# Kernel optimization log

Hardware: AMD Instinct MI355X
Metric: run time of the kernel (lower is better)

The kernel has to match this reference:

```python
import jax, jax.numpy as jnp
import numpy as np

S, B, D, E = 257, 64, 768, 8
H = 4 * D  # expert hidden dim

def quick_gelu(x):
    return x * jax.nn.sigmoid(1.702 * x)

def setup_inputs() -> dict:
    key = jax.random.key(0)
    ks = jax.random.split(key, 7)
    scale = 1.0 / np.sqrt(D)
    return {
        "x": jax.random.normal(ks[0], (S, B, D), dtype=jnp.float32),
        "W1": jax.random.normal(ks[1], (E, H, D), dtype=jnp.float32) * scale,   # fc1 weight per expert (out,in)
        "b1": jax.random.normal(ks[2], (E, H), dtype=jnp.float32) * 0.01,
        "W2": jax.random.normal(ks[3], (E, D, H), dtype=jnp.float32) * (1.0 / np.sqrt(H)),
        "b2": jax.random.normal(ks[4], (E, D), dtype=jnp.float32) * 0.01,
        "Wr": jax.random.normal(ks[5], (E, D), dtype=jnp.float32) * scale,       # router weight (E, d)
        "br": jnp.zeros((E,), dtype=jnp.float32),
    }

def reference(x, W1, b1, W2, b2, Wr, br):
    s, b, d = x.shape
    xf = x.reshape(s * b, d)                                  # [T, d]
    logits = xf @ Wr.T + br                                   # [T, E]
    probs = jax.nn.softmax(logits, axis=-1)                   # [T, E]
    # all-experts MLP, batched over the expert axis
    h = jnp.einsum('td,ehd->teh', xf, W1) + b1                # [T, E, 4d]
    h = quick_gelu(h)
    outs = jnp.einsum('teh,edh->ted', h, W2) + b2             # [T, E, d]
    y = jnp.einsum('ted,te->td', outs, probs)                 # router-weighted combine
    return y.reshape(s, b, d)
```

## Files before the change

kernel.cpp:

```cpp
#include <hip/hip_runtime.h>

typedef unsigned short u16;
typedef float f32x4 __attribute__((ext_vector_type(4)));
typedef short s16x8 __attribute__((ext_vector_type(8)));

#define T_TOK   16448L
#define D_DIM   768L
#define H_DIM   3072L
#define E_NUM   8L
#define M_PAD   16512L

__device__ __forceinline__ u16 f2bf(float f){
  unsigned u = __float_as_uint(f);
  u = u + 0x7FFFu + ((u >> 16) & 1u);
  return (u16)(u >> 16);
}
__device__ __forceinline__ unsigned f2bf2(float a, float b){
  return (unsigned)f2bf(a) | ((unsigned)f2bf(b) << 16);
}

__device__ __forceinline__ void gload_lds16(const u16* g, u16* s){
  __builtin_amdgcn_global_load_lds((const __attribute__((address_space(1))) void*)g,
                                   (__attribute__((address_space(3))) void*)s,
                                   16, 0, 0);
}

__device__ __forceinline__ int xcd_chunk(int idx, int n){
  const int q = n >> 3, r = n & 7, x = idx & 7;
  return (x < r ? x*(q+1) : r*(q+1) + (x-r)*q) + (idx >> 3);
}

__global__ void k_conv(const float* __restrict__ in, u16* __restrict__ outp,
                       long nValid, long nTotal){
  long i = (long)blockIdx.x * blockDim.x + threadIdx.x;
  long stride = (long)gridDim.x * blockDim.x;
  long n8 = nTotal >> 3;
  for (long v = i; v < n8; v += stride){
    long base = v << 3;
    uint4 o;
    if (base < nValid){
      const float4 f0 = *(const float4*)(in + base);
      const float4 f1 = *(const float4*)(in + base + 4);
      o.x = f2bf2(f0.x, f0.y); o.y = f2bf2(f0.z, f0.w);
      o.z = f2bf2(f1.x, f1.y); o.w = f2bf2(f1.z, f1.w);
    } else {
      o.x = 0u; o.y = 0u; o.z = 0u; o.w = 0u;
    }
    *(uint4*)(outp + base) = o;
  }
}

__global__ void k_router(const float* __restrict__ x, const float* __restrict__ Wr,
                         const float* __restrict__ br, float* __restrict__ probs){
  int w = (int)((blockIdx.x * (long)blockDim.x + threadIdx.x) >> 6);
  int lane = threadIdx.x & 63;
  if (w >= (int)T_TOK) return;
  const float* xr = x + (long)w * D_DIM;
  float l[8];
#pragma unroll
  for (int e = 0; e < 8; ++e) l[e] = 0.f;
#pragma unroll
  for (int c = 0; c < 3; ++c){
    const float4 xv = *(const float4*)(xr + c*256 + lane*4);
#pragma unroll
    for (int e = 0; e < 8; ++e){
      const float4 wv = *(const float4*)(Wr + (long)e*D_DIM + c*256 + lane*4);
      l[e] += xv.x*wv.x + xv.y*wv.y + xv.z*wv.z + xv.w*wv.w;
    }
  }
#pragma unroll
  for (int e = 0; e < 8; ++e){
#pragma unroll
    for (int off = 32; off > 0; off >>= 1) l[e] += __shfl_xor(l[e], off);
    l[e] += br[e];
  }
  float m = l[0];
#pragma unroll
  for (int e = 1; e < 8; ++e) m = fmaxf(m, l[e]);
  float s = 0.f;
#pragma unroll
  for (int e = 0; e < 8; ++e){ l[e] = __expf(l[e] - m); s += l[e]; }
  float inv = 1.f / s;
  if (lane == 0){
    float4 p0 = { l[0]*inv, l[1]*inv, l[2]*inv, l[3]*inv };
    float4 p1 = { l[4]*inv, l[5]*inv, l[6]*inv, l[7]*inv };
    *(float4*)(probs + (long)w*8)     = p0;
    *(float4*)(probs + (long)w*8 + 4) = p1;
  }
}

__device__ __forceinline__ void gemm128(const u16* __restrict__ Ag, long lda,
                                        const u16* __restrict__ Bg, long ldb,
                                        int NT, u16* As, u16* Bs,
                                        int tid, f32x4 (&acc)[4][4]){
  const int l  = tid & 63, w = tid >> 6;
  const int wr = w >> 1,  wc = w & 1;
  const int g4 = l >> 4,  ln = l & 15;

  const int rw = l >> 3;
  const int c8 = (l & 7) ^ rw;
  const u16* pA = Ag + (long)(w*8 + rw) * lda + c8*8;
  const u16* pB = Bg + (long)(w*8 + rw) * ldb + c8*8;
  const long sA = 32 * lda, sB = 32 * ldb;
  u16* dA = As + w*512;
  u16* dB = Bs + w*512;

  int offA[2][4], offB[2][4];
#pragma unroll
  for (int kk = 0; kk < 2; ++kk)
#pragma unroll
    for (int i = 0; i < 4; ++i){
      const int co = (((kk<<2) | g4) ^ (ln & 7)) << 3;
      offA[kk][i] = (wr*64 + i*16 + ln)*64 + co;
      offB[kk][i] = (wc*64 + i*16 + ln)*64 + co;
    }

  for (int kt = 0; kt < NT; ++kt){
    gload_lds16(pA,        dA);
    gload_lds16(pA +   sA, dA + 2048);
    gload_lds16(pA + 2*sA, dA + 4096);
    gload_lds16(pA + 3*sA, dA + 6144);
    gload_lds16(pB,        dB);
    gload_lds16(pB +   sB, dB + 2048);
    gload_lds16(pB + 2*sB, dB + 4096);
    gload_lds16(pB + 3*sB, dB + 6144);
    pA += 64; pB += 64;
    __syncthreads();

    s16x8 a0[4], b0[4], a1[4], b1[4];
#pragma unroll
    for (int i = 0; i < 4; ++i) a0[i] = *(const s16x8*)(As + offA[0][i]);
#pragma unroll
    for (int i = 0; i < 4; ++i) b0[i] = *(const s16x8*)(Bs + offB[0][i]);
#pragma unroll
    for (int mi = 0; mi < 4; ++mi)
#pragma unroll
      for (int ni = 0; ni < 4; ++ni)
        acc[mi][ni] = __builtin_amdgcn_mfma_f32_16x16x32_bf16(a0[mi], b0[ni], acc[mi][ni], 0, 0, 0);
#pragma unroll
    for (int i = 0; i < 4; ++i) a1[i] = *(const s16x8*)(As + offA[1][i]);
#pragma unroll
    for (int i = 0; i < 4; ++i) b1[i] = *(const s16x8*)(Bs + offB[1][i]);
#pragma unroll
    for (int mi = 0; mi < 4; ++mi)
#pragma unroll
      for (int ni = 0; ni < 4; ++ni)
        acc[mi][ni] = __builtin_amdgcn_mfma_f32_16x16x32_bf16(a1[mi], b1[ni], acc[mi][ni], 0, 0, 0);
    __syncthreads();
  }
}

__global__ __launch_bounds__(256) void k_pair(const u16* __restrict__ xb,
                                              const u16* __restrict__ w1b,
                                              const float* __restrict__ b1,
                                              const u16* __restrict__ w2b,
                                              const float* __restrict__ b2,
                                              const float* __restrict__ probs,
                                              float* __restrict__ out,
                                              const u16* __restrict__ hbR,
                                              u16* __restrict__ hbW,
                                              int e2, int t02,
                                              int e1, int t01, int mt1, int n2){
  __shared__ alignas(16) u16 As[8192];
  __shared__ alignas(16) u16 Bs[8192];
  const int tid = threadIdx.x;
  const int l  = tid & 63, w = tid >> 6;
  const int wr = w >> 1,  wc = w & 1;
  const int g4 = l >> 4,  ln = l & 15;
  const int bx = (int)blockIdx.x;
  f32x4 acc[4][4] = {};

  if (bx < n2){
    const int wg = xcd_chunk(bx, n2);
    const int tx = wg / 6, ty = wg % 6;
    const int m0 = tx << 7, n0 = ty << 7;
    gemm128(hbR + (long)m0 * H_DIM, H_DIM,
            w2b + ((long)e2 * D_DIM + n0) * H_DIM, H_DIM,
            48, As, Bs, tid, acc);
    float bias[4];
#pragma unroll
    for (int ni = 0; ni < 4; ++ni) bias[ni] = b2[(long)e2*D_DIM + n0 + wc*64 + ni*16 + ln];
#pragma unroll
    for (int mi = 0; mi < 4; ++mi){
#pragma unroll
      for (int j = 0; j < 4; ++j){
        const int gt = t02 + m0 + wr*64 + mi*16 + g4*4 + j;
        if (gt < (int)T_TOK){
          const float p = probs[(long)gt*8 + e2];
          float* dst = out + (long)gt * D_DIM + n0 + wc*64;
#pragma unroll
          for (int ni = 0; ni < 4; ++ni){
            const float v = p * (acc[mi][ni][j] + bias[ni]);
            if (e2 == 0) dst[ni*16 + ln] = v;
            else         dst[ni*16 + ln] += v;
          }
        }
      }
    }
  } else {
    const int n1 = (int)gridDim.x - n2;
    const int wg = xcd_chunk(bx - n2, n1);
    const int tx = wg % mt1, ty = wg / mt1;
    const int m0 = tx << 7, n0 = ty << 7;
    gemm128(xb + (long)(t01 + m0) * D_DIM, D_DIM,
            w1b + ((long)e1 * H_DIM + n0) * D_DIM, D_DIM,
            12, As, Bs, tid, acc);
    float bias[4];
#pragma unroll
    for (int ni = 0; ni < 4; ++ni) bias[ni] = b1[(long)e1*H_DIM + n0 + wc*64 + ni*16 + ln];
#pragma unroll
    for (int mi = 0; mi < 4; ++mi){
#pragma unroll
      for (int j = 0; j < 4; ++j){
        const int r = m0 + wr*64 + mi*16 + g4*4 + j;
        u16* dst = hbW + (long)r * H_DIM + n0 + wc*64;
#pragma unroll
        for (int ni = 0; ni < 4; ++ni){
          const float v  = acc[mi][ni][j] + bias[ni];
          const float gl = v / (1.0f + __expf(-1.702f * v));
          dst[ni*16 + ln] = f2bf(gl);
        }
      }
    }
  }
}

extern "C" void kernel_launch(void* const* d_in, const int* in_sizes, int n_in,
                              void* d_out, int out_size, void* d_ws, size_t ws_size,
                              hipStream_t stream){
  const float* x  = (const float*)d_in[0];
  const float* W1 = (const float*)d_in[1];
  const float* b1 = (const float*)d_in[2];
  const float* W2 = (const float*)d_in[3];
  const float* b2 = (const float*)d_in[4];
  const float* Wr = (const float*)d_in[5];
  const float* br = (const float*)d_in[6];
  float* out = (float*)d_out;

  char* ws = (char*)d_ws;
  size_t off = 0;
  auto carve = [&](size_t bytes)->void*{
    void* p = ws + off; off += (bytes + 255) & ~(size_t)255; return p;
  };
  u16*   xb    = (u16*)  carve((size_t)M_PAD * D_DIM * 2);
  u16*   w1b   = (u16*)  carve((size_t)E_NUM * H_DIM * D_DIM * 2);
  u16*   w2b   = (u16*)  carve((size_t)E_NUM * D_DIM * H_DIM * 2);
  float* probs = (float*)carve((size_t)T_TOK * E_NUM * 4);
  u16*   hbA   = (u16*)  carve((size_t)8192 * H_DIM * 2);
  u16*   hbB   = (u16*)  carve((size_t)8320 * H_DIM * 2);

  k_conv<<<dim3(2048), dim3(256), 0, stream>>>(x,  xb,  T_TOK*D_DIM, M_PAD*D_DIM);
  k_conv<<<dim3(2048), dim3(256), 0, stream>>>(W1, w1b, E_NUM*H_DIM*D_DIM, E_NUM*H_DIM*D_DIM);
  k_conv<<<dim3(2048), dim3(256), 0, stream>>>(W2, w2b, E_NUM*D_DIM*H_DIM, E_NUM*D_DIM*H_DIM);
  k_router<<<dim3(4112), dim3(256), 0, stream>>>(x, Wr, br, probs);

  const int MTA = 64, MTB = 65;
  const int T0A = 0,  T0B = 8192;

  auto pair = [&](int e2, const u16* hbR, int t02, int mt2,
                  int e1, u16* hbW, int t01, int mt1){
    const int n2 = mt2 * 6, n1 = mt1 * 24;
    k_pair<<<dim3((unsigned)(n2 + n1)), dim3(256), 0, stream>>>(
        xb, w1b, b1, w2b, b2, probs, out, hbR, hbW,
        e2, t02, e1, t01, mt1, n2);
  };

  pair(0, nullptr, 0, 0, 0, hbA, T0A, MTA);
  for (int e = 0; e < 8; ++e){
    pair(e, hbA, T0A, MTA, e, hbB, T0B, MTB);
    if (e < 7) pair(e, hbB, T0B, MTB, e + 1, hbA, T0A, MTA);
  }
  pair(7, hbB, T0B, MTB, 0, nullptr, 0, 0);
}
```

Before: 2.110 ms.

## Replace per-expert kernel launches with persistent megakernel using atomic flag dependencies

Merges the sequence of 17 paired GEMM launches into one large grid. Blocks are ordered by expert and role, and they wait on global atomic counters: fc1 waits until the previous expert's fc2 has finished reading the buffer, fc2 waits for fc1 to complete, and per-tile tickets order the output accumulation. A new init kernel zeroes the output and the flags. The aim is to remove launch gaps and tail idle time between kernels so the two phases overlap. The cost is spin-waiting, a dependence on blocks being dispatched in order (deadlock risk otherwise), and serialized output read-modify-write.

After: 4.271 ms. +102.4%, slower.

```diff
diff --git a/kernel.cpp b/kernel.cpp
--- a/kernel.cpp
+++ b/kernel.cpp
@@ -10,6 +10,12 @@
 #define E_NUM   8L
 #define M_PAD   16512L
 
+#define G1A 1536
+#define G2A 384
+#define G1B 1560
+#define G2B 390
+#define PE  3872
+
 __device__ __forceinline__ u16 f2bf(float f){
   unsigned u = __float_as_uint(f);
   u = u + 0x7FFFu + ((u >> 16) & 1u);
@@ -28,6 +34,35 @@
 __device__ __forceinline__ int xcd_chunk(int idx, int n){
   const int q = n >> 3, r = n & 7, x = idx & 7;
   return (x < r ? x*(q+1) : r*(q+1) + (x-r)*q) + (idx >> 3);
+}
+
+__device__ __forceinline__ void spin_ge(const int* p, int need){
+  if (threadIdx.x == 0){
+    while (__hip_atomic_load(p, __ATOMIC_RELAXED, __HIP_MEMORY_SCOPE_AGENT) < need)
+      __builtin_amdgcn_s_sleep(16);
+  }
+  __syncthreads();
+  __builtin_amdgcn_fence(__ATOMIC_ACQUIRE, "agent");
+}
+__device__ __forceinline__ void spin_eq(const int* p, int want){
+  if (threadIdx.x == 0){
+    while (__hip_atomic_load(p, __ATOMIC_RELAXED, __HIP_MEMORY_SCOPE_AGENT) != want)
+      __builtin_amdgcn_s_sleep(16);
+  }
+  __syncthreads();
+  __builtin_amdgcn_fence(__ATOMIC_ACQUIRE, "agent");
+}
+__device__ __forceinline__ void signal_add(int* p){
+  __syncthreads();
+  if (threadIdx.x == 0)
+    __hip_atomic_fetch_add(p, 1, __ATOMIC_RELEASE, __HIP_MEMORY_SCOPE_AGENT);
+}
+
+__global__ void k_init(float* __restrict__ out, long n, int* __restrict__ flags, int nf){
+  long i = (long)blockIdx.x * blockDim.x + threadIdx.x;
+  long st = (long)gridDim.x * blockDim.x;
+  for (long v = i; v < n; v += st) out[v] = 0.f;
+  for (long v = i; v < nf; v += st) flags[v] = 0;
 }
 
 __global__ void k_conv(const float* __restrict__ in, u16* __restrict__ outp,
@@ -150,70 +185,57 @@
   }
 }
 
-__global__ __launch_bounds__(256) void k_pair(const u16* __restrict__ xb,
+__global__ __launch_bounds__(256) void k_mega(const u16* __restrict__ xb,
                                               const u16* __restrict__ w1b,
                                               const float* __restrict__ b1,
                                               const u16* __restrict__ w2b,
                                               const float* __restrict__ b2,
                                               const float* __restrict__ probs,
                                               float* __restrict__ out,
-                                              const u16* __restrict__ hbR,
-                                              u16* __restrict__ hbW,
-                                              int e2, int t02,
-                                              int e1, int t01, int mt1, int n2){
+                                              u16* __restrict__ hbA,
+                                              u16* __restrict__ hbB,
+                                              int* __restrict__ flags){
   __shared__ alignas(16) u16 As[8192];
   __shared__ alignas(16) u16 Bs[8192];
   const int tid = threadIdx.x;
   const int l  = tid & 63, w = tid >> 6;
   const int wr = w >> 1,  wc = w & 1;
   const int g4 = l >> 4,  ln = l & 15;
-  const int bx = (int)blockIdx.x;
+
+  const int e = (int)blockIdx.x / PE;
+  const int r = (int)blockIdx.x % PE;
+  if (r >= 3870) return;
+  int* cnt    = flags;
+  int* gdone  = flags + 16;
+  int* ticket = flags + 32;
+
+  int role, half, wg;
+  if      (r < G1A)            { role = 1; half = 0; wg = xcd_chunk(r, G1A); }
+  else if (r < G1A+G2A)        { role = 2; half = 0; wg = xcd_chunk(r - G1A, G2A); }
+  else if (r < G1A+G2A+G1B)    { role = 1; half = 1; wg = xcd_chunk(r - G1A - G2A, G1B); }
+  else                         { role = 2; half = 1; wg = xcd_chunk(r - G1A - G2A - G1B, G2B); }
+
   f32x4 acc[4][4] = {};
 
-  if (bx < n2){
-    const int wg = xcd_chunk(bx, n2);
-    const int tx = wg / 6, ty = wg % 6;
-    const int m0 = tx << 7, n0 = ty << 7;
-    gemm128(hbR + (long)m0 * H_DIM, H_DIM,
-            w2b + ((long)e2 * D_DIM + n0) * H_DIM, H_DIM,
-            48, As, Bs, tid, acc);
-    float bias[4];
-#pragma unroll
-    for (int ni = 0; ni < 4; ++ni) bias[ni] = b2[(long)e2*D_DIM + n0 + wc*64 + ni*16 + ln];
-#pragma unroll
-    for (int mi = 0; mi < 4; ++mi){
-#pragma unroll
-      for (int j = 0; j < 4; ++j){
-        const int gt = t02 + m0 + wr*64 + mi*16 + g4*4 + j;
-        if (gt < (int)T_TOK){
-          const float p = probs[(long)gt*8 + e2];
-          float* dst = out + (long)gt * D_DIM + n0 + wc*64;
-#pragma unroll
-          for (int ni = 0; ni < 4; ++ni){
-            const float v = p * (acc[mi][ni][j] + bias[ni]);
-            if (e2 == 0) dst[ni*16 + ln] = v;
-            else         dst[ni*16 + ln] += v;
-          }
-        }
-      }
-    }
-  } else {
-    const int n1 = (int)gridDim.x - n2;
-    const int wg = xcd_chunk(bx - n2, n1);
+  if (role == 1){
+    const int mt1 = half ? 65 : 64;
+    const int t01 = half ? 8192 : 0;
+    u16* hbW = half ? hbB : hbA;
     const int tx = wg % mt1, ty = wg / mt1;
     const int m0 = tx << 7, n0 = ty << 7;
+    if (e > 0) spin_ge(&gdone[(e-1)*2 + half], half ? G2B : G2A);
     gemm128(xb + (long)(t01 + m0) * D_DIM, D_DIM,
-            w1b + ((long)e1 * H_DIM + n0) * D_DIM, D_DIM,
+            w1b + ((long)e * H_DIM + n0) * D_DIM, D_DIM,
             12, As, Bs, tid, acc);
     float bias[4];
 #pragma unroll
-    for (int ni = 0; ni < 4; ++ni) bias[ni] = b1[(long)e1*H_DIM + n0 + wc*64 + ni*16 + ln];
+    for (int ni = 0; ni < 4; ++ni) bias[ni] = b1[(long)e*H_DIM + n0 + wc*64 + ni*16 + ln];
 #pragma unroll
     for (int mi = 0; mi < 4; ++mi){
 #pragma unroll
       for (int j = 0; j < 4; ++j){
-        const int r = m0 + wr*64 + mi*16 + g4*4 + j;
-        u16* dst = hbW + (long)r * H_DIM + n0 + wc*64;
+        const int rr = m0 + wr*64 + mi*16 + g4*4 + j;
+        u16* dst = hbW + (long)rr * H_DIM + n0 + wc*64;
 #pragma unroll
         for (int ni = 0; ni < 4; ++ni){
           const float v  = acc[mi][ni][j] + bias[ni];
@@ -222,6 +244,40 @@
         }
       }
     }
+    signal_add(&cnt[e*2 + half]);
+  } else {
+    const int mt2 = half ? 65 : 64;
+    const int t02 = half ? 8192 : 0;
+    const u16* hbR = half ? hbB : hbA;
+    const int tx = wg / 6, ty = wg % 6;
+    const int m0 = tx << 7, n0 = ty << 7;
+    spin_ge(&cnt[e*2 + half], half ? G1B : G1A);
+    gemm128(hbR + (long)m0 * H_DIM, H_DIM,
+            w2b + ((long)e * D_DIM + n0) * H_DIM, H_DIM,
+            48, As, Bs, tid, acc);
+    signal_add(&gdone[e*2 + half]);
+    float bias[4];
+#pragma unroll
+    for (int ni = 0; ni < 4; ++ni) bias[ni] = b2[(long)e*D_DIM + n0 + wc*64 + ni*16 + ln];
+    const int tk = (half ? G2A : 0) + tx*6 + ty;
+    spin_eq(&ticket[tk], e);
+#pragma unroll
+    for (int mi = 0; mi < 4; ++mi){
+#pragma unroll
+      for (int j = 0; j < 4; ++j){
+        const int gt = t02 + m0 + wr*64 + mi*16 + g4*4 + j;
+        if (gt < (int)T_TOK){
+          const float p = probs[(long)gt*8 + e];
+          float* dst = out + (long)gt * D_DIM + n0 + wc*64;
+#pragma unroll
+          for (int ni = 0; ni < 4; ++ni)
+            dst[ni*16 + ln] += p * (acc[mi][ni][j] + bias[ni]);
+        }
+      }
+    }
+    __syncthreads();
+    if (tid == 0)
+      __hip_atomic_store(&ticket[tk], e + 1, __ATOMIC_RELEASE, __HIP_MEMORY_SCOPE_AGENT);
   }
 }
 
@@ -248,27 +304,14 @@
   float* probs = (float*)carve((size_t)T_TOK * E_NUM * 4);
   u16*   hbA   = (u16*)  carve((size_t)8192 * H_DIM * 2);
   u16*   hbB   = (u16*)  carve((size_t)8320 * H_DIM * 2);
-
+  int*   flags = (int*)  carve(4096);
+
+  k_init<<<dim3(1024), dim3(256), 0, stream>>>(out, (long)out_size, flags, 1024);
   k_conv<<<dim3(2048), dim3(256), 0, stream>>>(x,  xb,  T_TOK*D_DIM, M_PAD*D_DIM);
   k_conv<<<dim3(2048), dim3(256), 0, stream>>>(W1, w1b, E_NUM*H_DIM*D_DIM, E_NUM*H_DIM*D_DIM);
   k_conv<<<dim3(2048), dim3(256), 0, stream>>>(W2, w2b, E_NUM*D_DIM*H_DIM, E_NUM*D_DIM*H_DIM);
   k_router<<<dim3(4112), dim3(256), 0, stream>>>(x, Wr, br, probs);
 
-  const int MTA = 64, MTB = 65;
-  const int T0A = 0,  T0B = 8192;
-
-  auto pair = [&](int e2, const u16* hbR, int t02, int mt2,
-                  int e1, u16* hbW, int t01, int mt1){
-    const int n2 = mt2 * 6, n1 = mt1 * 24;
-    k_pair<<<dim3((unsigned)(n2 + n1)), dim3(256), 0, stream>>>(
-        xb, w1b, b1, w2b, b2, probs, out, hbR, hbW,
-        e2, t02, e1, t01, mt1, n2);
-  };
-
-  pair(0, nullptr, 0, 0, 0, hbA, T0A, MTA);
-  for (int e = 0; e < 8; ++e){
-    pair(e, hbA, T0A, MTA, e, hbB, T0B, MTB);
-    if (e < 7) pair(e, hbB, T0B, MTB, e + 1, hbA, T0A, MTA);
-  }
-  pair(7, hbB, T0B, MTB, 0, nullptr, 0, 0);
-}
+  k_mega<<<dim3((unsigned)(E_NUM * PE)), dim3(256), 0, stream>>>(
+      xb, w1b, b1, w2b, b2, probs, out, hbA, hbB, flags);
+}
```

## Split-K the fc2 GEMM into two halves with a partial buffer and final reduce

Applied to the files above, without the earlier changes.

The fc2 GEMM inside each pair launch is split along the hidden dimension into two K-halves. This doubles the fc2 workgroup count and halves each workgroup's K loop, so the long fc2 tiles no longer dominate the tail of each paired launch. The second half accumulates into a separate fp32 partial buffer across experts, and a final reduce kernel adds it into the output. The cost is an extra 50MB partial buffer with its read-modify-write traffic plus one more kernel launch.

Measured after the change: 2.351 ms. 1.11x slower.

```diff
diff --git a/kernel.cpp b/kernel.cpp
--- a/kernel.cpp
+++ b/kernel.cpp
@@ -89,6 +89,18 @@
   }
 }
 
+__global__ void k_reduce(float* __restrict__ out, const float* __restrict__ part1,
+                         long n4){
+  long i = (long)blockIdx.x * blockDim.x + threadIdx.x;
+  long st = (long)gridDim.x * blockDim.x;
+  for (long v = i; v < n4; v += st){
+    float4 a = *(const float4*)(out + (v<<2));
+    const float4 b = *(const float4*)(part1 + (v<<2));
+    a.x += b.x; a.y += b.y; a.z += b.z; a.w += b.w;
+    *(float4*)(out + (v<<2)) = a;
+  }
+}
+
 __device__ __forceinline__ void gemm128(const u16* __restrict__ Ag, long lda,
                                         const u16* __restrict__ Bg, long ldb,
                                         int NT, u16* As, u16* Bs,
@@ -157,9 +169,10 @@
                                               const float* __restrict__ b2,
                                               const float* __restrict__ probs,
                                               float* __restrict__ out,
+                                              float* __restrict__ part1,
                                               const u16* __restrict__ hbR,
                                               u16* __restrict__ hbW,
-                                              int e2, int t02,
+                                              int e2, int t02, int mt2,
                                               int e1, int t01, int mt1, int n2){
   __shared__ alignas(16) u16 As[8192];
   __shared__ alignas(16) u16 Bs[8192];
@@ -171,15 +184,20 @@
   f32x4 acc[4][4] = {};
 
   if (bx < n2){
-    const int wg = xcd_chunk(bx, n2);
-    const int tx = wg / 6, ty = wg % 6;
+    const int wg  = xcd_chunk(bx, n2);
+    const int per = mt2 * 6;
+    const int sp  = wg / per;
+    const int rem = wg % per;
+    const int tx = rem / 6, ty = rem % 6;
     const int m0 = tx << 7, n0 = ty << 7;
-    gemm128(hbR + (long)m0 * H_DIM, H_DIM,
-            w2b + ((long)e2 * D_DIM + n0) * H_DIM, H_DIM,
-            48, As, Bs, tid, acc);
+    gemm128(hbR + (long)m0 * H_DIM + sp*1536, H_DIM,
+            w2b + ((long)e2 * D_DIM + n0) * H_DIM + sp*1536, H_DIM,
+            24, As, Bs, tid, acc);
     float bias[4];
 #pragma unroll
-    for (int ni = 0; ni < 4; ++ni) bias[ni] = b2[(long)e2*D_DIM + n0 + wc*64 + ni*16 + ln];
+    for (int ni = 0; ni < 4; ++ni)
+      bias[ni] = sp ? 0.f : b2[(long)e2*D_DIM + n0 + wc*64 + ni*16 + ln];
+    float* dstBuf = sp ? part1 : out;
 #pragma unroll
     for (int mi = 0; mi < 4; ++mi){
 #pragma unroll
@@ -187,7 +205,7 @@
         const int gt = t02 + m0 + wr*64 + mi*16 + g4*4 + j;
         if (gt < (int)T_TOK){
           const float p = probs[(long)gt*8 + e2];
-          float* dst = out + (long)gt * D_DIM + n0 + wc*64;
+          float* dst = dstBuf + (long)gt * D_DIM + n0 + wc*64;
 #pragma unroll
           for (int ni = 0; ni < 4; ++ni){
             const float v = p * (acc[mi][ni][j] + bias[ni]);
@@ -248,6 +266,7 @@
   float* probs = (float*)carve((size_t)T_TOK * E_NUM * 4);
   u16*   hbA   = (u16*)  carve((size_t)8192 * H_DIM * 2);
   u16*   hbB   = (u16*)  carve((size_t)8320 * H_DIM * 2);
+  float* part1 = (float*)carve((size_t)T_TOK * D_DIM * 4);
 
   k_conv<<<dim3(2048), dim3(256), 0, stream>>>(x,  xb,  T_TOK*D_DIM, M_PAD*D_DIM);
   k_conv<<<dim3(2048), dim3(256), 0, stream>>>(W1, w1b, E_NUM*H_DIM*D_DIM, E_NUM*H_DIM*D_DIM);
@@ -259,10 +278,11 @@
 
   auto pair = [&](int e2, const u16* hbR, int t02, int mt2,
                   int e1, u16* hbW, int t01, int mt1){
-    const int n2 = mt2 * 6, n1 = mt1 * 24;
+    const int n2 = mt2 * 12;
+    const int n1 = mt1 * 24;
     k_pair<<<dim3((unsigned)(n2 + n1)), dim3(256), 0, stream>>>(
-        xb, w1b, b1, w2b, b2, probs, out, hbR, hbW,
-        e2, t02, e1, t01, mt1, n2);
+        xb, w1b, b1, w2b, b2, probs, out, part1, hbR, hbW,
+        e2, t02, mt2, e1, t01, mt1, n2);
   };
 
   pair(0, nullptr, 0, 0, 0, hbA, T0A, MTA);
@@ -271,4 +291,6 @@
     if (e < 7) pair(e, hbB, T0B, MTB, e + 1, hbA, T0A, MTA);
   }
   pair(7, hbB, T0B, MTB, 0, nullptr, 0, 0);
-}
+
+  k_reduce<<<dim3(2048), dim3(256), 0, stream>>>(out, part1, (T_TOK * D_DIM) >> 2);
+}
```
